# Kernel tuning notes

Hardware: AMD Instinct MI355X
Metric: run time of the kernel (lower is better)

Reference implementation:

```python
import jax, jax.numpy as jnp
import numpy as np

IN_FEATURES = 8192
OUT_FEATURES = 4096
NNZ = 4194304
N_COLS = 4096  # must equal OUT_FEATURES so torch's bias broadcast is valid


def setup_inputs() -> dict:
    key = jax.random.key(0)
    k1, k2, k3, k4, k5 = jax.random.split(key, 5)
    values = jax.random.normal(k1, (NNZ,), dtype=jnp.float32)
    bias = jax.random.normal(k2, (OUT_FEATURES,), dtype=jnp.float32)
    x = jax.random.normal(k3, (OUT_FEATURES, N_COLS), dtype=jnp.float32)
    rows = jax.random.randint(k4, (NNZ,), 0, IN_FEATURES, dtype=jnp.int32)
    cols = jax.random.randint(k5, (NNZ,), 0, OUT_FEATURES, dtype=jnp.int32)
    return {"values": values, "bias": bias, "x": x, "rows": rows, "cols": cols}


def reference(values, bias, x, rows, cols):
    # Densify the COO sparse weight; duplicate coordinates are summed,
    # matching torch.sparse COO semantics.
    W = jnp.zeros((IN_FEATURES, OUT_FEATURES), dtype=x.dtype).at[rows, cols].add(values)
    # torch.sparse.addmm(bias, W, x) = bias + W @ x
    # result: [IN_FEATURES, N_COLS]; bias [OUT_FEATURES] broadcasts over the
    # last axis (valid because N_COLS == OUT_FEATURES, as in the original).
    return bias + W @ x
```

## Files before the change

kernel.cpp:

```cpp
#include <hip/hip_runtime.h>

#define M_DIM 8192
#define K_DIM 4096
#define N_DIM 4096
#define NNZ_CNT 4194304
#define GRID_X 16
#define GRID_Y 32

#define BINS 2048
#define BIN_ROWS 4
#define NBLK 512
#define CHUNK 8192
#define RSV 24
#define TRANS_BLKS 4096

typedef __attribute__((ext_vector_type(8))) short bf16x8;
typedef __attribute__((ext_vector_type(4))) float f32x4;

__device__ __forceinline__ unsigned short f2bf(float f) {
  unsigned int u = __float_as_uint(f);
  unsigned int r = (u + 0x7FFFu + ((u >> 16) & 1u)) >> 16;
  return (unsigned short)r;
}

__device__ __forceinline__ unsigned int pack2(float a, float b) {
  return (unsigned int)f2bf(a) | ((unsigned int)f2bf(b) << 16);
}

__device__ __forceinline__ void gload_lds16(const void* g, void* l) {
  __builtin_amdgcn_global_load_lds(
      (const __attribute__((address_space(1))) void*)g,
      (__attribute__((address_space(3))) void*)l, 16, 0, 0);
}

__global__ __launch_bounds__(256) void fused_pre(
    const float* __restrict__ vals,
    const int* __restrict__ rows,
    const int* __restrict__ cols,
    unsigned int* __restrict__ packets,
    unsigned int* __restrict__ counts,
    const float* __restrict__ x,
    unsigned short* __restrict__ xT) {
  __shared__ __align__(16) char smraw[64 * 65 * 4];
  const int tid = threadIdx.x;

  if (blockIdx.x < NBLK) {
    unsigned int* lcur = (unsigned int*)smraw;
    const int blk = blockIdx.x;
#pragma unroll 8
    for (int b = tid; b < BINS; b += 256) lcur[b] = 0;
    __syncthreads();
    const int base = blk * CHUNK;
    const int4* r4 = (const int4*)(rows + base);
    const int4* c4 = (const int4*)(cols + base);
    const float4* v4 = (const float4*)(vals + base);
    unsigned int* wnd = packets + (long)blk * BINS * RSV;
#pragma unroll 2
    for (int it = 0; it < CHUNK / 4 / 256; ++it) {
      int idx = it * 256 + tid;
      int4 r = r4[idx];
      int4 c = c4[idx];
      float4 v = v4[idx];
#pragma unroll
      for (int e = 0; e < 4; ++e) {
        int rr = (&r.x)[e], cc = (&c.x)[e];
        float vv = (&v.x)[e];
        unsigned int pk = (unsigned int)f2bf(vv) |
                          ((unsigned int)cc << 16) |
                          ((unsigned int)(rr & (BIN_ROWS - 1)) << 28);
        int bin = rr >> 2;
        unsigned int slot = atomicAdd(&lcur[bin], 1u);
        if (slot < RSV) wnd[(unsigned)bin * RSV + slot] = pk;
      }
    }
    __syncthreads();
#pragma unroll 8
    for (int b = tid; b < BINS; b += 256)
      counts[blk * BINS + b] = lcur[b];
  } else {
    float (*tile)[65] = (float(*)[65])smraw;
    const int t = blockIdx.x - NBLK;
    const int nb = (t & 63) * 64;
    const int kb = (t >> 6) * 64;
    const int tx = tid & 15;
    const int ty = tid >> 4;
#pragma unroll
    for (int i = 0; i < 4; ++i) {
      const int k = ty + 16 * i;
      float4 v = *(const float4*)&x[(long)(kb + k) * N_DIM + nb + 4 * tx];
      tile[k][4 * tx + 0] = v.x; tile[k][4 * tx + 1] = v.y;
      tile[k][4 * tx + 2] = v.z; tile[k][4 * tx + 3] = v.w;
    }
    __syncthreads();
#pragma unroll
    for (int i = 0; i < 4; ++i) {
      const int n = ty + 16 * i;
      ushort4 o;
      o.x = f2bf(tile[4 * tx + 0][n]);
      o.y = f2bf(tile[4 * tx + 1][n]);
      o.z = f2bf(tile[4 * tx + 2][n]);
      o.w = f2bf(tile[4 * tx + 3][n]);
      *(ushort4*)&xT[(long)(nb + n) * K_DIM + kb + 4 * tx] = o;
    }
  }
}

__global__ __launch_bounds__(256) void apply_bins(
    const unsigned int* __restrict__ packets,
    const unsigned int* __restrict__ counts,
    unsigned int* __restrict__ Wb2) {
  extern __shared__ float acc[];
  const int bin = blockIdx.x;
  const int tid = threadIdx.x;
  float4* a4 = (float4*)acc;
#pragma unroll 4
  for (int i = tid; i < BIN_ROWS * K_DIM / 4; i += 256)
    a4[i] = float4{0.f, 0.f, 0.f, 0.f};
  __syncthreads();
#pragma unroll
  for (int half = 0; half < 2; ++half) {
    const int blk = tid + half * 256;
    unsigned int cnt = counts[blk * BINS + bin];
    if (cnt > RSV) cnt = RSV;
    const uint4* seg4 = (const uint4*)(packets + ((long)blk * BINS + bin) * RSV);
    for (unsigned int v = 0; v * 4 < cnt; ++v) {
      uint4 pkv = seg4[v];
#pragma unroll
      for (int e = 0; e < 4; ++e) {
        unsigned int i = v * 4 + e;
        if (i < cnt) {
          unsigned int pk = (&pkv.x)[e];
          float val = __uint_as_float(pk << 16);
          int c = (pk >> 16) & 0xFFF;
          int r2 = pk >> 28;
          atomicAdd(&acc[r2 * K_DIM + c], val);
        }
      }
    }
  }
  __syncthreads();
  uint4* dst4 = (uint4*)(Wb2 + (long)bin * (BIN_ROWS * K_DIM / 2));
#pragma unroll 4
  for (int i = tid; i < BIN_ROWS * K_DIM / 8; i += 256) {
    float4 lo = a4[2 * i], hi = a4[2 * i + 1];
    uint4 o;
    o.x = pack2(lo.x, lo.y); o.y = pack2(lo.z, lo.w);
    o.z = pack2(hi.x, hi.y); o.w = pack2(hi.z, hi.w);
    dst4[i] = o;
  }
}


#define LDS_BUF   65536
#define LDS_B_OFF 32768

template<bool STA, bool STB, bool FIN>
__device__ __forceinline__ void tile_body(
    int u, int cur,
    const unsigned short* __restrict__ Ag, const unsigned short* __restrict__ Bg,
    char* smem, int st16,
    int a_off0, int a_off1, int b_off0, int b_off1,
    bf16x8 (&a)[4][2], bf16x8 (&b)[4][2], f32x4 (&acc)[8][4]) {
  char* Acur = smem + cur * LDS_BUF;
  char* Bcur = Acur + LDS_B_OFF;
  char* Aoth = smem + (cur ^ 1) * LDS_BUF;
  const unsigned short* Asrc = Ag + (long)(u + 1) * 64;
  const unsigned short* Bsrc = Bg + (long)(u + 2) * 64;

#pragma unroll
  for (int m = 0; m < 4; ++m) {
    a[m][0] = *(const bf16x8*)(Acur + m * 2048 + a_off0);
    a[m][1] = *(const bf16x8*)(Acur + m * 2048 + a_off1);
  }
#pragma unroll
  for (int n = 0; n < 2; ++n) {
    b[n][0] = *(const bf16x8*)(Bcur + n * 2048 + b_off0);
    b[n][1] = *(const bf16x8*)(Bcur + n * 2048 + b_off1);
  }
  if (STA) {
    gload_lds16(Asrc, Aoth + st16);
    gload_lds16(Asrc + (long)64 * K_DIM, Aoth + 8192 + st16);
  }
  __builtin_amdgcn_s_barrier();
  asm volatile("s_waitcnt lgkmcnt(0)" ::: "memory");
  __builtin_amdgcn_sched_barrier(0);
  __builtin_amdgcn_s_setprio(1);
#pragma unroll
  for (int m = 0; m < 4; ++m)
#pragma unroll
    for (int n = 0; n < 2; ++n) {
      acc[m][n] = __builtin_amdgcn_mfma_f32_16x16x32_bf16(a[m][0], b[n][0], acc[m][n], 0, 0, 0);
      acc[m][n] = __builtin_amdgcn_mfma_f32_16x16x32_bf16(a[m][1], b[n][1], acc[m][n], 0, 0, 0);
    }
  __builtin_amdgcn_s_setprio(0);
  __builtin_amdgcn_s_barrier();

#pragma unroll
  for (int n = 2; n < 4; ++n) {
    b[n][0] = *(const bf16x8*)(Bcur + n * 2048 + b_off0);
    b[n][1] = *(const bf16x8*)(Bcur + n * 2048 + b_off1);
  }
  if (STA) {
    gload_lds16(Asrc + (long)128 * K_DIM, Aoth + 16384 + st16);
    gload_lds16(Asrc + (long)192 * K_DIM, Aoth + 24576 + st16);
  }
  __builtin_amdgcn_s_barrier();
  asm volatile("s_waitcnt lgkmcnt(0)" ::: "memory");
  __builtin_amdgcn_sched_barrier(0);
  __builtin_amdgcn_s_setprio(1);
#pragma unroll
  for (int m = 0; m < 4; ++m)
#pragma unroll
    for (int n = 2; n < 4; ++n) {
      acc[m][n] = __builtin_amdgcn_mfma_f32_16x16x32_bf16(a[m][0], b[n][0], acc[m][n], 0, 0, 0);
      acc[m][n] = __builtin_amdgcn_mfma_f32_16x16x32_bf16(a[m][1], b[n][1], acc[m][n], 0, 0, 0);
    }
  __builtin_amdgcn_s_setprio(0);
  __builtin_amdgcn_s_barrier();

#pragma unroll
  for (int m = 0; m < 4; ++m) {
    a[m][0] = *(const bf16x8*)(Acur + (m + 4) * 2048 + a_off0);
    a[m][1] = *(const bf16x8*)(Acur + (m + 4) * 2048 + a_off1);
  }
  if (STB) {
    gload_lds16(Bsrc, Bcur + st16);
    gload_lds16(Bsrc + (long)64 * K_DIM, Bcur + 8192 + st16);
  }
  __builtin_amdgcn_s_barrier();
  asm volatile("s_waitcnt lgkmcnt(0)" ::: "memory");
  __builtin_amdgcn_sched_barrier(0);
  __builtin_amdgcn_s_setprio(1);
#pragma unroll
  for (int m = 0; m < 4; ++m)
#pragma unroll
    for (int n = 0; n < 2; ++n) {
      acc[m + 4][n] = __builtin_amdgcn_mfma_f32_16x16x32_bf16(a[m][0], b[n][0], acc[m + 4][n], 0, 0, 0);
      acc[m + 4][n] = __builtin_amdgcn_mfma_f32_16x16x32_bf16(a[m][1], b[n][1], acc[m + 4][n], 0, 0, 0);
    }
  __builtin_amdgcn_s_setprio(0);
  __builtin_amdgcn_s_barrier();

  if (STB) {
    gload_lds16(Bsrc + (long)128 * K_DIM, Bcur + 16384 + st16);
    gload_lds16(Bsrc + (long)192 * K_DIM, Bcur + 24576 + st16);
  }
  if (FIN) asm volatile("s_waitcnt vmcnt(0)" ::: "memory");
  else     asm volatile("s_waitcnt vmcnt(4)" ::: "memory");
  __builtin_amdgcn_s_barrier();
  __builtin_amdgcn_s_setprio(1);
#pragma unroll
  for (int m = 0; m < 4; ++m)
#pragma unroll
    for (int n = 2; n < 4; ++n) {
      acc[m + 4][n] = __builtin_amdgcn_mfma_f32_16x16x32_bf16(a[m][0], b[n][0], acc[m + 4][n], 0, 0, 0);
      acc[m + 4][n] = __builtin_amdgcn_mfma_f32_16x16x32_bf16(a[m][1], b[n][1], acc[m + 4][n], 0, 0, 0);
    }
  __builtin_amdgcn_s_setprio(0);
  __builtin_amdgcn_s_barrier();
}

__global__ __launch_bounds__(512, 2) void gemm8(
    const unsigned short* __restrict__ A,
    const unsigned short* __restrict__ B,
    const float* __restrict__ bias,
    float* __restrict__ C) {
  extern __shared__ __align__(16) char smem[];
  const int tid = threadIdx.x;
  const int lane = tid & 63;
  const int wid = tid >> 6;
  const int wr = wid >> 2, wc = wid & 3;

  const int wg0 = blockIdx.y * GRID_X + blockIdx.x;
  const int swz = (wg0 & 7) * (GRID_X * GRID_Y / 8) + (wg0 >> 3);
  const int bm0 = (swz >> 4) * 256;
  const int bn0 = (swz & 15) * 256;

  const int srow = tid >> 3;
  const int pcb = (tid & 7) << 4;
  const int scol = (pcb ^ ((srow & 7) << 4)) >> 1;
  const unsigned short* Ag = A + (long)(bm0 + srow) * K_DIM + scol;
  const unsigned short* Bg = B + (long)(bn0 + srow) * K_DIM + scol;
  const int st16 = tid * 16;

  const int q = (lane >> 4) << 4;
  const int s = (lane & 7) << 4;
  const int qs = q ^ s;
  const int a_off0 = (wr * 128 + (lane & 15)) * 128 + qs;
  const int a_off1 = a_off0 ^ 64;
  const int b_off0 = (wc * 64 + (lane & 15)) * 128 + qs;
  const int b_off1 = b_off0 ^ 64;

  f32x4 acc[8][4] = {};
  bf16x8 a[4][2], b[4][2];

#pragma unroll
  for (int h = 0; h < 2; ++h)
#pragma unroll
    for (int r = 0; r < 2; ++r) {
      gload_lds16(Ag + (long)(h * 128 + r * 64) * K_DIM,
                  smem + h * 16384 + r * 8192 + st16);
      gload_lds16(Bg + (long)(h * 128 + r * 64) * K_DIM,
                  smem + LDS_B_OFF + h * 16384 + r * 8192 + st16);
    }
#pragma unroll
  for (int h = 0; h < 2; ++h)
#pragma unroll
    for (int r = 0; r < 2; ++r)
      gload_lds16(Bg + (long)(h * 128 + r * 64) * K_DIM + 64,
                  smem + LDS_BUF + LDS_B_OFF + h * 16384 + r * 8192 + st16);
  asm volatile("s_waitcnt vmcnt(4)" ::: "memory");
  __builtin_amdgcn_s_barrier();

#pragma unroll 1
  for (int u2 = 0; u2 < 31; ++u2) {
    tile_body<true, true, false>(2 * u2, 0, Ag, Bg, smem, st16,
                                 a_off0, a_off1, b_off0, b_off1, a, b, acc);
    tile_body<true, true, false>(2 * u2 + 1, 1, Ag, Bg, smem, st16,
                                 a_off0, a_off1, b_off0, b_off1, a, b, acc);
  }
  tile_body<true, false, true>(62, 0, Ag, Bg, smem, st16,
                               a_off0, a_off1, b_off0, b_off1, a, b, acc);
  tile_body<false, false, true>(63, 1, Ag, Bg, smem, st16,
                                a_off0, a_off1, b_off0, b_off1, a, b, acc);

#pragma unroll
  for (int n = 0; n < 4; ++n) {
    const int col = bn0 + wc * 64 + n * 16 + (lane & 15);
    const float bv = bias[col];
#pragma unroll
    for (int m = 0; m < 8; ++m) {
      const int r0 = bm0 + wr * 128 + m * 16 + (lane >> 4) * 4;
#pragma unroll
      for (int j = 0; j < 4; ++j)
        C[(long)(r0 + j) * N_DIM + col] = acc[m][n][j] + bv;
    }
  }
}

extern "C" void kernel_launch(void* const* d_in, const int* in_sizes, int n_in,
                              void* d_out, int out_size, void* d_ws, size_t ws_size,
                              hipStream_t stream) {
  const float* values = (const float*)d_in[0];
  const float* bias   = (const float*)d_in[1];
  const float* x      = (const float*)d_in[2];
  const int*   rows   = (const int*)d_in[3];
  const int*   cols   = (const int*)d_in[4];
  float* out = (float*)d_out;

  unsigned short* Wb = (unsigned short*)d_ws;
  unsigned short* xT = (unsigned short*)((char*)d_ws + (size_t)M_DIM * K_DIM * 2);

  unsigned int* packets = (unsigned int*)d_out;
  unsigned int* counts = (unsigned int*)((char*)d_out + (112u << 20));

  hipFuncSetAttribute((const void*)gemm8,
                      hipFuncAttributeMaxDynamicSharedMemorySize, 131072);
  hipFuncSetAttribute((const void*)apply_bins,
                      hipFuncAttributeMaxDynamicSharedMemorySize, 65536);

  fused_pre<<<NBLK + TRANS_BLKS, 256, 0, stream>>>(values, rows, cols,
                                                   packets, counts, x, xT);
  apply_bins<<<BINS, 256, 65536, stream>>>(packets, counts, (unsigned int*)Wb);
  gemm8<<<dim3(GRID_X, GRID_Y), 512, 131072, stream>>>(Wb, xT, bias, out);
}
```

Baseline: 337.3 us.

## Prefetch A two tiles ahead into current buffer alongside B loads

Changes the GEMM software pipeline so A tiles are prefetched two k-steps ahead into the current LDS buffer at the end of each tile, matching B's prefetch distance, instead of one step ahead into the other buffer. The prologue now preloads two full A/B stages, and the vmcnt wait is raised to allow eight outstanding loads. This is meant to give A global loads more time in flight and to simplify the schedule. In exchange, all A loads are bunched after the last LDS read, which may increase memory burstiness and reduce how far the load issue is spread across the tile.

```diff
diff --git a/kernel.cpp b/kernel.cpp
--- a/kernel.cpp
+++ b/kernel.cpp
@@ -154,7 +154,7 @@
 #define LDS_BUF   65536
 #define LDS_B_OFF 32768
 
-template<bool STA, bool STB, bool FIN>
+template<bool ST, bool FIN>
 __device__ __forceinline__ void tile_body(
     int u, int cur,
     const unsigned short* __restrict__ Ag, const unsigned short* __restrict__ Bg,
@@ -163,8 +163,7 @@
     bf16x8 (&a)[4][2], bf16x8 (&b)[4][2], f32x4 (&acc)[8][4]) {
   char* Acur = smem + cur * LDS_BUF;
   char* Bcur = Acur + LDS_B_OFF;
-  char* Aoth = smem + (cur ^ 1) * LDS_BUF;
-  const unsigned short* Asrc = Ag + (long)(u + 1) * 64;
+  const unsigned short* Asrc = Ag + (long)(u + 2) * 64;
   const unsigned short* Bsrc = Bg + (long)(u + 2) * 64;
 
 #pragma unroll
@@ -177,10 +176,6 @@
     b[n][0] = *(const bf16x8*)(Bcur + n * 2048 + b_off0);
     b[n][1] = *(const bf16x8*)(Bcur + n * 2048 + b_off1);
   }
-  if (STA) {
-    gload_lds16(Asrc, Aoth + st16);
-    gload_lds16(Asrc + (long)64 * K_DIM, Aoth + 8192 + st16);
-  }
   __builtin_amdgcn_s_barrier();
   asm volatile("s_waitcnt lgkmcnt(0)" ::: "memory");
   __builtin_amdgcn_sched_barrier(0);
@@ -200,10 +195,6 @@
     b[n][0] = *(const bf16x8*)(Bcur + n * 2048 + b_off0);
     b[n][1] = *(const bf16x8*)(Bcur + n * 2048 + b_off1);
   }
-  if (STA) {
-    gload_lds16(Asrc + (long)128 * K_DIM, Aoth + 16384 + st16);
-    gload_lds16(Asrc + (long)192 * K_DIM, Aoth + 24576 + st16);
-  }
   __builtin_amdgcn_s_barrier();
   asm volatile("s_waitcnt lgkmcnt(0)" ::: "memory");
   __builtin_amdgcn_sched_barrier(0);
@@ -223,7 +214,7 @@
     a[m][0] = *(const bf16x8*)(Acur + (m + 4) * 2048 + a_off0);
     a[m][1] = *(const bf16x8*)(Acur + (m + 4) * 2048 + a_off1);
   }
-  if (STB) {
+  if (ST) {
     gload_lds16(Bsrc, Bcur + st16);
     gload_lds16(Bsrc + (long)64 * K_DIM, Bcur + 8192 + st16);
   }
@@ -241,12 +232,15 @@
   __builtin_amdgcn_s_setprio(0);
   __builtin_amdgcn_s_barrier();
 
-  if (STB) {
+  if (ST) {
     gload_lds16(Bsrc + (long)128 * K_DIM, Bcur + 16384 + st16);
     gload_lds16(Bsrc + (long)192 * K_DIM, Bcur + 24576 + st16);
+#pragma unroll
+    for (int r = 0; r < 4; ++r)
+      gload_lds16(Asrc + (long)(r * 64) * K_DIM, Acur + r * 8192 + st16);
   }
   if (FIN) asm volatile("s_waitcnt vmcnt(0)" ::: "memory");
-  else     asm volatile("s_waitcnt vmcnt(4)" ::: "memory");
+  else     asm volatile("s_waitcnt vmcnt(8)" ::: "memory");
   __builtin_amdgcn_s_barrier();
   __builtin_amdgcn_s_setprio(1);
 #pragma unroll
@@ -295,34 +289,28 @@
   bf16x8 a[4][2], b[4][2];
 
 #pragma unroll
-  for (int h = 0; h < 2; ++h)
-#pragma unroll
-    for (int r = 0; r < 2; ++r) {
-      gload_lds16(Ag + (long)(h * 128 + r * 64) * K_DIM,
-                  smem + h * 16384 + r * 8192 + st16);
-      gload_lds16(Bg + (long)(h * 128 + r * 64) * K_DIM,
-                  smem + LDS_B_OFF + h * 16384 + r * 8192 + st16);
-    }
-#pragma unroll
-  for (int h = 0; h < 2; ++h)
-#pragma unroll
-    for (int r = 0; r < 2; ++r)
-      gload_lds16(Bg + (long)(h * 128 + r * 64) * K_DIM + 64,
-                  smem + LDS_BUF + LDS_B_OFF + h * 16384 + r * 8192 + st16);
-  asm volatile("s_waitcnt vmcnt(4)" ::: "memory");
+  for (int t = 0; t < 2; ++t)
+#pragma unroll
+    for (int r = 0; r < 4; ++r) {
+      gload_lds16(Ag + (long)t * 64 + (long)(r * 64) * K_DIM,
+                  smem + t * LDS_BUF + r * 8192 + st16);
+      gload_lds16(Bg + (long)t * 64 + (long)(r * 64) * K_DIM,
+                  smem + t * LDS_BUF + LDS_B_OFF + r * 8192 + st16);
+    }
+  asm volatile("s_waitcnt vmcnt(8)" ::: "memory");
   __builtin_amdgcn_s_barrier();
 
 #pragma unroll 1
   for (int u2 = 0; u2 < 31; ++u2) {
-    tile_body<true, true, false>(2 * u2, 0, Ag, Bg, smem, st16,
-                                 a_off0, a_off1, b_off0, b_off1, a, b, acc);
-    tile_body<true, true, false>(2 * u2 + 1, 1, Ag, Bg, smem, st16,
-                                 a_off0, a_off1, b_off0, b_off1, a, b, acc);
-  }
-  tile_body<true, false, true>(62, 0, Ag, Bg, smem, st16,
-                               a_off0, a_off1, b_off0, b_off1, a, b, acc);
-  tile_body<false, false, true>(63, 1, Ag, Bg, smem, st16,
-                                a_off0, a_off1, b_off0, b_off1, a, b, acc);
+    tile_body<true, false>(2 * u2, 0, Ag, Bg, smem, st16,
+                           a_off0, a_off1, b_off0, b_off1, a, b, acc);
+    tile_body<true, false>(2 * u2 + 1, 1, Ag, Bg, smem, st16,
+                           a_off0, a_off1, b_off0, b_off1, a, b, acc);
+  }
+  tile_body<false, true>(62, 0, Ag, Bg, smem, st16,
+                         a_off0, a_off1, b_off0, b_off1, a, b, acc);
+  tile_body<false, true>(63, 1, Ag, Bg, smem, st16,
+                         a_off0, a_off1, b_off0, b_off1, a, b, acc);
 
 #pragma unroll
   for (int n = 0; n < 4; ++n) {
```

Result: slower. 360.7 us (+6.9%).
